# Kernel optimization log

Hardware: AMD Instinct MI355X
Metric: run time of the kernel (lower is better)

Reference implementation:

```python
import jax, jax.numpy as jnp
import numpy as np

D_IN = 512
EMBED = 256
N = 8192

def setup_inputs() -> dict:
    key = jax.random.key(0)
    ks = jax.random.split(key, 6)
    s_in = 1.0 / np.sqrt(D_IN)
    s_e = 1.0 / np.sqrt(EMBED)
    return {
        "X": jax.random.normal(ks[0], (N, D_IN), dtype=jnp.float32),
        "W_Q": jax.random.uniform(ks[1], (EMBED, D_IN), jnp.float32, -s_in, s_in),
        "W_K": jax.random.uniform(ks[2], (EMBED, D_IN), jnp.float32, -s_in, s_in),
        "W_V": jax.random.uniform(ks[3], (EMBED, D_IN), jnp.float32, -s_in, s_in),
        "head_w": jax.random.uniform(ks[4], (1, EMBED), jnp.float32, -s_e, s_e),
        "head_b": jax.random.uniform(ks[5], (1,), jnp.float32, -s_e, s_e),
    }

def reference(X, W_Q, W_K, W_V, head_w, head_b):
    # Projections: nn.Linear(x) = x @ W.T
    Q = X @ W_Q.T                      # [N, D]
    K = X @ W_K.T                      # [N, D]
    V = X @ W_V.T                      # [N, D]
    A = Q @ K.T                        # [N, N] unnormalized linear attention
    Z = A @ V                          # [N, D]
    preds = Z @ head_w.T + head_b      # [N, 1]
    return preds[:, 0]                 # [N]
```

## Files before the change

kernel.cpp:

```cpp
#include <hip/hip_runtime.h>

typedef unsigned long long ull;

#define D_IN 512
#define EMBED 256
#define NBLK 256
#define SCALE 16777216.0f
#define INV_SCALE 5.9604644775390625e-08f
#define AG __HIP_MEMORY_SCOPE_AGENT

#define WS_TFX 0
#define WS_CNT 32768
#define WS_WVP 32832
#define WS_RP  49216
#define WS_RV  114752
#define N_ZERO 4104

__device__ __forceinline__ void fstore_cg(float* p, float v) {
    __hip_atomic_store((unsigned*)p, __builtin_bit_cast(unsigned, v),
                       __ATOMIC_RELAXED, AG);
}
__device__ __forceinline__ float fload_cg(const float* p) {
    unsigned u = __hip_atomic_load((const unsigned*)p, __ATOMIC_RELAXED, AG);
    return __builtin_bit_cast(float, u);
}
__device__ __forceinline__ ull uload_cg(const ull* p) {
    return __hip_atomic_load(p, __ATOMIC_RELAXED, AG);
}

__global__ __launch_bounds__(512) void k_prep(const float* __restrict__ W_V,
                                              const float* __restrict__ head_w,
                                              float* __restrict__ wvp,
                                              ull* __restrict__ z) {
    const int j   = blockIdx.x;
    const int tid = threadIdx.x;
    float acc = 0.f;
    const int e0 = j * 32;
#pragma unroll 8
    for (int m = 0; m < 32; ++m)
        acc += head_w[e0 + m] * W_V[(size_t)(e0 + m) * D_IN + tid];
    wvp[(size_t)j * D_IN + tid] = acc;

    for (int i = j * 512 + tid; i < N_ZERO; i += 8 * 512) z[i] = 0ull;
}

__global__ __launch_bounds__(512) void k_fused2(
    const float* __restrict__ X,
    const float* __restrict__ W_Q,
    const float* __restrict__ W_K,
    const float* __restrict__ head_b,
    float* __restrict__ out,
    char* __restrict__ ws)
{
    ull*   t_fixed = (ull*)(ws + WS_TFX);
    ull*   cnts    = (ull*)(ws + WS_CNT);
    ull*   t_cnt   = cnts + 0;
    ull*   rp_cnt  = cnts + 1;
    ull*   r_done  = cnts + 2;
    const float* wvp = (const float*)(ws + WS_WVP);
    float* rp      = (float*)(ws + WS_RP);
    float* rv      = (float*)(ws + WS_RV);

    const int b    = blockIdx.x;
    const int tid  = threadIdx.x;
    const int lane = tid & 63;
    const int wid  = tid >> 6;
    const int c0   = lane * 4;
    const int c1   = 256 + lane * 4;

    __shared__ float lds[8][D_IN];
    __shared__ float t_lds[D_IN];
    __shared__ float rv_lds[D_IN];
    __shared__ float u_lds[8];
    __shared__ unsigned flag_s;

    float4 xa[4], xb[4];
    const int row0 = b * 32 + wid * 4;
#pragma unroll
    for (int r = 0; r < 4; ++r) {
        const float* xr = X + (size_t)(row0 + r) * D_IN;
        xa[r] = *(const float4*)(xr + c0);
        xb[r] = *(const float4*)(xr + c1);
    }

    float4 wv0 = {0.f,0.f,0.f,0.f}, wv1 = {0.f,0.f,0.f,0.f};
#pragma unroll
    for (int j = 0; j < 8; ++j) {
        const float4 a = *(const float4*)(wvp + (size_t)j * D_IN + c0);
        const float4 bq = *(const float4*)(wvp + (size_t)j * D_IN + c1);
        wv0.x += a.x;  wv0.y += a.y;  wv0.z += a.z;  wv0.w += a.w;
        wv1.x += bq.x; wv1.y += bq.y; wv1.z += bq.z; wv1.w += bq.w;
    }

    float4 t0 = {0.f,0.f,0.f,0.f};
    float4 t1 = {0.f,0.f,0.f,0.f};
#pragma unroll
    for (int r = 0; r < 4; ++r) {
        float p = xa[r].x*wv0.x + xa[r].y*wv0.y + xa[r].z*wv0.z + xa[r].w*wv0.w
                + xb[r].x*wv1.x + xb[r].y*wv1.y + xb[r].z*wv1.z + xb[r].w*wv1.w;
#pragma unroll
        for (int off = 32; off >= 1; off >>= 1) p += __shfl_xor(p, off, 64);
        t0.x += p*xa[r].x; t0.y += p*xa[r].y; t0.z += p*xa[r].z; t0.w += p*xa[r].w;
        t1.x += p*xb[r].x; t1.y += p*xb[r].y; t1.z += p*xb[r].z; t1.w += p*xb[r].w;
    }
    *(float4*)(&lds[wid][c0]) = t0;
    *(float4*)(&lds[wid][c1]) = t1;
    __syncthreads();
    {
        float s = 0.f;
#pragma unroll
        for (int w = 0; w < 8; ++w) s += lds[w][tid];
        const long long v = llrintf(s * SCALE);
        ull old = atomicAdd(&t_fixed[(size_t)(b & 7) * D_IN + tid], (ull)v);
        unsigned keep = (unsigned)old ^ (unsigned)(old >> 32);
        asm volatile("" :: "v"(keep));
    }
    __syncthreads();

    if (tid == 0) flag_s = (unsigned)atomicAdd(t_cnt, 1ull);
    __syncthreads();
    const unsigned arrival = flag_s;

    if (arrival >= 224u) {
        const int k = (int)arrival - 224;
        if (tid == 0) {
            while (atomicAdd(t_cnt, 0ull) < 256ull) __builtin_amdgcn_s_sleep(8);
        }
        __syncthreads();

        long long acc = 0;
#pragma unroll
        for (int j = 0; j < 8; ++j)
            acc += (long long)atomicAdd(&t_fixed[(size_t)j * D_IN + tid], 0ull);
        t_lds[tid] = (float)acc * INV_SCALE;
        __syncthreads();

        {
            const int e = 8 * k + wid;
            const float4 ta = *(const float4*)(t_lds + c0);
            const float4 tb = *(const float4*)(t_lds + c1);
            const float4 ka = *(const float4*)(W_K + (size_t)e * D_IN + c0);
            const float4 kb = *(const float4*)(W_K + (size_t)e * D_IN + c1);
            float p = ta.x*ka.x + ta.y*ka.y + ta.z*ka.z + ta.w*ka.w
                    + tb.x*kb.x + tb.y*kb.y + tb.z*kb.z + tb.w*kb.w;
#pragma unroll
            for (int off = 32; off >= 1; off >>= 1) p += __shfl_xor(p, off, 64);
            if (lane == 0) u_lds[wid] = p;
        }
        __syncthreads();

        {
            float racc = 0.f;
#pragma unroll
            for (int m = 0; m < 8; ++m)
                racc += u_lds[m] * W_Q[(size_t)(8 * k + m) * D_IN + tid];
            fstore_cg(&rp[(size_t)k * D_IN + tid], racc);
        }
        __syncthreads();
        if (tid == 0) flag_s = ((unsigned)atomicAdd(rp_cnt, 1ull) == 31u) ? 1u : 0u;
        __syncthreads();

        if (flag_s) {
            float s = 0.f;
#pragma unroll 8
            for (int j = 0; j < 32; ++j) s += fload_cg(&rp[(size_t)j * D_IN + tid]);
            fstore_cg(&rv[tid], s);
            __syncthreads();
            if (tid == 0) atomicAdd(r_done, 1ull);
        }
    }

    if (tid == 0) {
        while (uload_cg(r_done) == 0ull) __builtin_amdgcn_s_sleep(4);
    }
    __syncthreads();

    if (tid < 256) {
        ull two = uload_cg((const ull*)rv + tid);
        rv_lds[2 * tid]     = __builtin_bit_cast(float, (unsigned)two);
        rv_lds[2 * tid + 1] = __builtin_bit_cast(float, (unsigned)(two >> 32));
    }
    __syncthreads();

    const float4 r0 = *(const float4*)(rv_lds + c0);
    const float4 r1 = *(const float4*)(rv_lds + c1);
    const float bb = head_b[0];

#pragma unroll
    for (int r = 0; r < 4; ++r) {
        float p = xa[r].x*r0.x + xa[r].y*r0.y + xa[r].z*r0.z + xa[r].w*r0.w
                + xb[r].x*r1.x + xb[r].y*r1.y + xb[r].z*r1.z + xb[r].w*r1.w;
#pragma unroll
        for (int off = 32; off >= 1; off >>= 1) p += __shfl_xor(p, off, 64);
        if (lane == 0) out[row0 + r] = p + bb;
    }
}

extern "C" void kernel_launch(void* const* d_in, const int* in_sizes, int n_in,
                              void* d_out, int out_size, void* d_ws, size_t ws_size,
                              hipStream_t stream) {
    const float* X      = (const float*)d_in[0];
    const float* W_Q    = (const float*)d_in[1];
    const float* W_K    = (const float*)d_in[2];
    const float* W_V    = (const float*)d_in[3];
    const float* head_w = (const float*)d_in[4];
    const float* head_b = (const float*)d_in[5];
    float* out = (float*)d_out;
    char* ws   = (char*)d_ws;

    float* wvp = (float*)(ws + WS_WVP);

    k_prep  <<<8,    512, 0, stream>>>(W_V, head_w, wvp, (ull*)ws);
    k_fused2<<<NBLK, 512, 0, stream>>>(X, W_Q, W_K, head_b, out, ws);
}
```

Before: 27.13 us.

## Replace r partial-sum stage with fixed-point atomics and drop X register caching

```diff
diff --git a/kernel.cpp b/kernel.cpp
--- a/kernel.cpp
+++ b/kernel.cpp
@@ -3,29 +3,30 @@
 typedef unsigned long long ull;
 
 #define D_IN 512
-#define EMBED 256
 #define NBLK 256
 #define SCALE 16777216.0f
 #define INV_SCALE 5.9604644775390625e-08f
 #define AG __HIP_MEMORY_SCOPE_AGENT
 
 #define WS_TFX 0
-#define WS_CNT 32768
-#define WS_WVP 32832
-#define WS_RP  49216
-#define WS_RV  114752
-#define N_ZERO 4104
+#define WS_RFX 32768
+#define WS_CNT 36864
+#define WS_WVP 40960
+#define N_ZERO 4616
 
 __device__ __forceinline__ void fstore_cg(float* p, float v) {
     __hip_atomic_store((unsigned*)p, __builtin_bit_cast(unsigned, v),
                        __ATOMIC_RELAXED, AG);
 }
-__device__ __forceinline__ float fload_cg(const float* p) {
-    unsigned u = __hip_atomic_load((const unsigned*)p, __ATOMIC_RELAXED, AG);
-    return __builtin_bit_cast(float, u);
-}
 __device__ __forceinline__ ull uload_cg(const ull* p) {
     return __hip_atomic_load(p, __ATOMIC_RELAXED, AG);
+}
+__device__ __forceinline__ ulonglong2 load_b128_coherent(const ull* p) {
+    ulonglong2 v;
+    asm volatile("global_load_dwordx4 %0, %1, off sc0 sc1\n\t"
+                 "s_waitcnt vmcnt(0)"
+                 : "=&v"(v) : "v"(p) : "memory");
+    return v;
 }
 
 __global__ __launch_bounds__(512) void k_prep(const float* __restrict__ W_V,
@@ -44,7 +45,7 @@
     for (int i = j * 512 + tid; i < N_ZERO; i += 8 * 512) z[i] = 0ull;
 }
 
-__global__ __launch_bounds__(512) void k_fused2(
+__global__ __launch_bounds__(512) void k_one(
     const float* __restrict__ X,
     const float* __restrict__ W_Q,
     const float* __restrict__ W_K,
@@ -53,13 +54,11 @@
     char* __restrict__ ws)
 {
     ull*   t_fixed = (ull*)(ws + WS_TFX);
+    ull*   r_fixed = (ull*)(ws + WS_RFX);
     ull*   cnts    = (ull*)(ws + WS_CNT);
     ull*   t_cnt   = cnts + 0;
-    ull*   rp_cnt  = cnts + 1;
-    ull*   r_done  = cnts + 2;
+    ull*   r_cnt   = cnts + 1;
     const float* wvp = (const float*)(ws + WS_WVP);
-    float* rp      = (float*)(ws + WS_RP);
-    float* rv      = (float*)(ws + WS_RV);
 
     const int b    = blockIdx.x;
     const int tid  = threadIdx.x;
@@ -70,23 +69,14 @@
 
     __shared__ float lds[8][D_IN];
     __shared__ float t_lds[D_IN];
-    __shared__ float rv_lds[D_IN];
+    __shared__ float r_lds[D_IN];
     __shared__ float u_lds[8];
     __shared__ unsigned flag_s;
 
-    float4 xa[4], xb[4];
-    const int row0 = b * 32 + wid * 4;
-#pragma unroll
-    for (int r = 0; r < 4; ++r) {
-        const float* xr = X + (size_t)(row0 + r) * D_IN;
-        xa[r] = *(const float4*)(xr + c0);
-        xb[r] = *(const float4*)(xr + c1);
-    }
-
     float4 wv0 = {0.f,0.f,0.f,0.f}, wv1 = {0.f,0.f,0.f,0.f};
 #pragma unroll
     for (int j = 0; j < 8; ++j) {
-        const float4 a = *(const float4*)(wvp + (size_t)j * D_IN + c0);
+        const float4 a  = *(const float4*)(wvp + (size_t)j * D_IN + c0);
         const float4 bq = *(const float4*)(wvp + (size_t)j * D_IN + c1);
         wv0.x += a.x;  wv0.y += a.y;  wv0.z += a.z;  wv0.w += a.w;
         wv1.x += bq.x; wv1.y += bq.y; wv1.z += bq.z; wv1.w += bq.w;
@@ -94,14 +84,18 @@
 
     float4 t0 = {0.f,0.f,0.f,0.f};
     float4 t1 = {0.f,0.f,0.f,0.f};
+    const int row0 = b * 32 + wid * 4;
 #pragma unroll
     for (int r = 0; r < 4; ++r) {
-        float p = xa[r].x*wv0.x + xa[r].y*wv0.y + xa[r].z*wv0.z + xa[r].w*wv0.w
-                + xb[r].x*wv1.x + xb[r].y*wv1.y + xb[r].z*wv1.z + xb[r].w*wv1.w;
+        const float* xr = X + (size_t)(row0 + r) * D_IN;
+        const float4 a  = *(const float4*)(xr + c0);
+        const float4 bq = *(const float4*)(xr + c1);
+        float p = a.x*wv0.x  + a.y*wv0.y  + a.z*wv0.z  + a.w*wv0.w
+                + bq.x*wv1.x + bq.y*wv1.y + bq.z*wv1.z + bq.w*wv1.w;
 #pragma unroll
         for (int off = 32; off >= 1; off >>= 1) p += __shfl_xor(p, off, 64);
-        t0.x += p*xa[r].x; t0.y += p*xa[r].y; t0.z += p*xa[r].z; t0.w += p*xa[r].w;
-        t1.x += p*xb[r].x; t1.y += p*xb[r].y; t1.z += p*xb[r].z; t1.w += p*xb[r].w;
+        t0.x += p*a.x;  t0.y += p*a.y;  t0.z += p*a.z;  t0.w += p*a.w;
+        t1.x += p*bq.x; t1.y += p*bq.y; t1.z += p*bq.z; t1.w += p*bq.w;
     }
     *(float4*)(&lds[wid][c0]) = t0;
     *(float4*)(&lds[wid][c1]) = t1;
@@ -124,14 +118,14 @@
     if (arrival >= 224u) {
         const int k = (int)arrival - 224;
         if (tid == 0) {
-            while (atomicAdd(t_cnt, 0ull) < 256ull) __builtin_amdgcn_s_sleep(8);
+            while (uload_cg(t_cnt) < 256ull) __builtin_amdgcn_s_sleep(1);
         }
         __syncthreads();
 
         long long acc = 0;
 #pragma unroll
         for (int j = 0; j < 8; ++j)
-            acc += (long long)atomicAdd(&t_fixed[(size_t)j * D_IN + tid], 0ull);
+            acc += (long long)uload_cg(&t_fixed[(size_t)j * D_IN + tid]);
         t_lds[tid] = (float)acc * INV_SCALE;
         __syncthreads();
 
@@ -154,42 +148,38 @@
 #pragma unroll
             for (int m = 0; m < 8; ++m)
                 racc += u_lds[m] * W_Q[(size_t)(8 * k + m) * D_IN + tid];
-            fstore_cg(&rp[(size_t)k * D_IN + tid], racc);
+            const long long v = llrintf(racc * SCALE);
+            ull old = atomicAdd(&r_fixed[tid], (ull)v);
+            unsigned keep = (unsigned)old ^ (unsigned)(old >> 32);
+            asm volatile("" :: "v"(keep));
         }
         __syncthreads();
-        if (tid == 0) flag_s = ((unsigned)atomicAdd(rp_cnt, 1ull) == 31u) ? 1u : 0u;
-        __syncthreads();
-
-        if (flag_s) {
-            float s = 0.f;
-#pragma unroll 8
-            for (int j = 0; j < 32; ++j) s += fload_cg(&rp[(size_t)j * D_IN + tid]);
-            fstore_cg(&rv[tid], s);
-            __syncthreads();
-            if (tid == 0) atomicAdd(r_done, 1ull);
-        }
+        if (tid == 0) atomicAdd(r_cnt, 1ull);
     }
 
     if (tid == 0) {
-        while (uload_cg(r_done) == 0ull) __builtin_amdgcn_s_sleep(4);
+        while (uload_cg(r_cnt) < 32ull) __builtin_amdgcn_s_sleep(2);
     }
     __syncthreads();
 
     if (tid < 256) {
-        ull two = uload_cg((const ull*)rv + tid);
-        rv_lds[2 * tid]     = __builtin_bit_cast(float, (unsigned)two);
-        rv_lds[2 * tid + 1] = __builtin_bit_cast(float, (unsigned)(two >> 32));
-    }
-    __syncthreads();
-
-    const float4 r0 = *(const float4*)(rv_lds + c0);
-    const float4 r1 = *(const float4*)(rv_lds + c1);
-    const float bb = head_b[0];
+        ulonglong2 v = load_b128_coherent(r_fixed + 2 * tid);
+        r_lds[2 * tid]     = (float)(long long)v.x * INV_SCALE;
+        r_lds[2 * tid + 1] = (float)(long long)v.y * INV_SCALE;
+    }
+    __syncthreads();
+
+    const float4 r0 = *(const float4*)(r_lds + c0);
+    const float4 r1 = *(const float4*)(r_lds + c1);
+    const float bb  = head_b[0];
 
 #pragma unroll
     for (int r = 0; r < 4; ++r) {
-        float p = xa[r].x*r0.x + xa[r].y*r0.y + xa[r].z*r0.z + xa[r].w*r0.w
-                + xb[r].x*r1.x + xb[r].y*r1.y + xb[r].z*r1.z + xb[r].w*r1.w;
+        const float* xr = X + (size_t)(row0 + r) * D_IN;
+        const float4 a  = *(const float4*)(xr + c0);
+        const float4 bq = *(const float4*)(xr + c1);
+        float p = a.x*r0.x  + a.y*r0.y  + a.z*r0.z  + a.w*r0.w
+                + bq.x*r1.x + bq.y*r1.y + bq.z*r1.z + bq.w*r1.w;
 #pragma unroll
         for (int off = 32; off >= 1; off >>= 1) p += __shfl_xor(p, off, 64);
         if (lane == 0) out[row0 + r] = p + bb;
@@ -210,6 +200,6 @@
 
     float* wvp = (float*)(ws + WS_WVP);
 
-    k_prep  <<<8,    512, 0, stream>>>(W_V, head_w, wvp, (ull*)ws);
-    k_fused2<<<NBLK, 512, 0, stream>>>(X, W_Q, W_K, head_b, out, ws);
-}
+    k_prep<<<8,    512, 0, stream>>>(W_V, head_w, wvp, (ull*)ws);
+    k_one <<<NBLK, 512, 0, stream>>>(X, W_Q, W_K, head_b, out, ws);
+}
```

Result: faster. 26.25 us (-3.2%).
